# Optimization experiments

Measured on AMD Instinct MI355X. Metric: run time of the kernel, lower is better.

## Reference

```python
import jax, jax.numpy as jnp
import numpy as np

RATE = 0.1
RANDOM_PORTION = 0.1


def setup_inputs() -> dict:
    key = jax.random.key(0)
    x = jax.random.normal(key, (32, 524288), dtype=jnp.float32)
    return {"x": x}


def reference(x) -> jnp.ndarray:
    # Training-mode forward of RandomTopKModifier.
    b = x.shape[0]
    xf = x.reshape(b, -1)                      # [B, N]
    n = xf.shape[1]
    k = max(1, round(RATE * n))

    # 1) top-k by magnitude (indices only; unsorted is fine, set-equivalent)
    _, topk_idx = jax.lax.top_k(jnp.abs(xf), k)            # [B, k] int32

    # 2) build per-element sampling probabilities:
    #    random_portion mass spread over the N-k non-topk slots,
    #    (1 - random_portion) mass spread over the k topk slots.
    rows = jnp.arange(b)[:, None]                           # [B, 1]
    probs = jnp.full_like(xf, RANDOM_PORTION / (n - k))
    probs = probs.at[rows, topk_idx].set((1.0 - RANDOM_PORTION) / k)

    # 3) weighted sampling of k indices WITHOUT replacement
    #    (torch.multinomial(probs, k)) via the Gumbel-top-k trick.
    g = jax.random.gumbel(jax.random.key(42), xf.shape, dtype=xf.dtype)
    _, sel_idx = jax.lax.top_k(jnp.log(probs) + g, k)       # [B, k]

    # 4) scatter a binary mask and apply it
    mask = jnp.zeros_like(xf).at[rows, sel_idx].set(1.0)
    return (mask * xf).reshape(x.shape)
```

## Files before the change

### kernel.cpp

```cpp
#include <hip/hip_runtime.h>
#include <stdint.h>


static constexpr uint32_t BB = 32;
static constexpr uint32_t NN = 524288;
static constexpr uint32_t KK = 52429;
static constexpr uint32_t W = 64;
static constexpr uint32_t CHUNK = NN / W;
static constexpr uint32_t SEGCAP1 = 1024;
static constexpr uint32_t CAP1 = W * SEGCAP1;
static constexpr uint32_t SEGCAP2 = 1280;
static constexpr uint32_t CAP2 = W * SEGCAP2;
static constexpr uint32_t SELCAP = 512;
static constexpr uint32_t SENT = 0xFFFFFFFFu;
static constexpr uint32_t T1KEY = 0x3FD00000u;

__device__ __forceinline__ float xla_logf(float xin) {
#pragma clang fp contract(off)
  float x = fmaxf(xin, __uint_as_float(0x00800000u));
  uint32_t bits = __float_as_uint(x);
  float e = (float)((int)(bits >> 23) - 126);
  x = __uint_as_float((bits & 0x807fffffu) | 0x3f000000u);
  bool mlt = x < 0.707106781186547524f;
  float tmp = mlt ? x : 0.0f;
  x = x - 1.0f;
  e = e - (mlt ? 1.0f : 0.0f);
  x = x + tmp;
  float x2 = x * x;
  float x3 = x2 * x;
  float y, y1, y2;
  y  = 7.0376836292E-2f * x + -1.1514610310E-1f;
  y1 = -1.2420140846E-1f * x + 1.4249322787E-1f;
  y2 = 2.0000714765E-1f * x + -2.4999993993E-1f;
  y  = y * x + 1.1676998740E-1f;
  y1 = y1 * x + -1.6668057665E-1f;
  y2 = y2 * x + 3.3333331174E-1f;
  y  = y * x3 + y1;
  y  = y * x3 + y2;
  y  = y * x3;
  y1 = e * -2.12194440e-4f;
  tmp = x2 * 0.5f;
  y = y + y1;
  x = x - tmp;
  y2 = e * 0.693359375f;
  x = x + y;
  x = x + y2;
  return x;
}

__device__ __forceinline__ float c_top_val()  { return xla_logf((float)((1.0 - 0.1) / 52429.0)); }
__device__ __forceinline__ float c_rand_val() { return xla_logf((float)(0.1 / 471859.0)); }

__device__ __forceinline__ uint32_t tf_bits(uint32_t i) {
  const uint32_t ks0 = 0u, ks1 = 42u, ks2 = 0x1BD11BDAu ^ 42u;
  uint32_t x0 = 0u + ks0;
  uint32_t x1 = i + ks1;
#define TFR(r) { x0 += x1; x1 = (x1 << (r)) | (x1 >> (32 - (r))); x1 ^= x0; }
  TFR(13) TFR(15) TFR(26) TFR(6)
  x0 += ks1; x1 += ks2 + 1u;
  TFR(17) TFR(29) TFR(16) TFR(24)
  x0 += ks2; x1 += ks0 + 2u;
  TFR(13) TFR(15) TFR(26) TFR(6)
  x0 += ks0; x1 += ks1 + 3u;
  TFR(17) TFR(29) TFR(16) TFR(24)
  x0 += ks1; x1 += ks2 + 4u;
  TFR(13) TFR(15) TFR(26) TFR(6)
  x0 += ks2; x1 += ks0 + 5u;
#undef TFR
  return x0 ^ x1;
}

__device__ __forceinline__ uint32_t key_x(float v) { return __float_as_uint(v) & 0x7fffffffu; }
__device__ __forceinline__ uint32_t key_s(float v) {
  uint32_t b = __float_as_uint(v);
  return (b & 0x80000000u) ? ~b : (b | 0x80000000u);
}


__global__ void __launch_bounds__(256)
k_candcoll1(const float* __restrict__ src,
            uint32_t* __restrict__ cidx, uint32_t* __restrict__ ckey) {
  __shared__ uint32_t lcnt;
  uint32_t row = blockIdx.y, seg = blockIdx.x;
  if (threadIdx.x == 0) lcnt = 0u;
  __syncthreads();
  uint32_t colbase = seg * CHUNK;
  uint32_t base = row * CAP1 + seg * SEGCAP1;
  const float4* p = (const float4*)(src + (size_t)row * NN + colbase);
  for (uint32_t j = threadIdx.x; j < CHUNK / 4; j += 256) {
    float4 v = p[j];
    float vv[4] = {v.x, v.y, v.z, v.w};
#pragma unroll
    for (int e = 0; e < 4; ++e) {
      uint32_t key = key_x(vv[e]);
      if (key >= T1KEY) {
        uint32_t li = atomicAdd(&lcnt, 1u);
        if (li < SEGCAP1) { cidx[base + li] = colbase + j * 4 + e; ckey[base + li] = key; }
      }
    }
  }
  __syncthreads();
  uint32_t c = (lcnt < SEGCAP1) ? lcnt : SEGCAP1;
  for (uint32_t j = c + threadIdx.x; j < SEGCAP1; j += 256) ckey[base + j] = SENT;
}

__device__ __forceinline__ void scan_hist(const uint32_t* lh, uint32_t* csA,
                                          uint32_t* sh, uint32_t kk, uint32_t t) {
  uint32_t s0 = 0;
  if (t < 256) {
#pragma unroll
    for (int j = 0; j < 8; ++j) s0 += lh[t * 8 + j];
    csA[t] = s0;
  }
  __syncthreads();
#pragma unroll
  for (uint32_t stp = 1; stp < 256; stp <<= 1) {
    uint32_t v = 0;
    if (t < 256 && t + stp < 256) v = csA[t + stp];
    __syncthreads();
    if (t < 256) csA[t] += v;
    __syncthreads();
  }
  if (t < 256) {
    uint32_t Sst = csA[t] - s0;
    if (Sst < kk && Sst + s0 >= kk) {
      uint32_t acc = Sst, bin = t * 8;
      for (int b2 = (int)t * 8 + 7; b2 >= (int)t * 8; --b2) {
        uint32_t hv = lh[b2];
        if (acc + hv >= kk) { bin = (uint32_t)b2; break; }
        acc += hv;
      }
      sh[0] = bin; sh[1] = kk - acc;
    }
  }
  __syncthreads();
}

__global__ void __launch_bounds__(1024)
k_select(const uint32_t* __restrict__ cidx, const uint32_t* __restrict__ ckey,
         uint32_t cap, uint32_t* __restrict__ st, uint32_t* __restrict__ sel) {
  __shared__ uint32_t lh[2048];
  __shared__ uint32_t csA[256];
  __shared__ uint32_t lkey[1024];
  __shared__ uint32_t lidx[1024];
  __shared__ uint32_t sh[8];
  uint32_t row = blockIdx.x;
  uint32_t t = threadIdx.x;
  const uint4* pk = (const uint4*)(ckey + (size_t)row * cap);
  for (uint32_t b = t; b < 2048; b += 1024) lh[b] = 0u;
  __syncthreads();
  for (uint32_t j0 = 0; j0 < cap / 4; j0 += 4 * 1024) {
    uint4 k4[4];
#pragma unroll
    for (int u = 0; u < 4; ++u) k4[u] = pk[j0 + u * 1024 + t];
#pragma unroll
    for (int u = 0; u < 4; ++u) {
      uint32_t kk[4] = {k4[u].x, k4[u].y, k4[u].z, k4[u].w};
#pragma unroll
      for (int e = 0; e < 4; ++e)
        if (kk[e] != SENT) atomicAdd(&lh[kk[e] >> 21], 1u);
    }
  }
  __syncthreads();
  scan_hist(lh, csA, sh, KK, t);
  uint32_t b0 = sh[0], kk1 = sh[1];
  __syncthreads();
  for (uint32_t b = t; b < 2048; b += 1024) lh[b] = 0u;
  __syncthreads();
  for (uint32_t j0 = 0; j0 < cap / 4; j0 += 4 * 1024) {
    uint4 k4[4];
#pragma unroll
    for (int u = 0; u < 4; ++u) k4[u] = pk[j0 + u * 1024 + t];
#pragma unroll
    for (int u = 0; u < 4; ++u) {
      uint32_t kk[4] = {k4[u].x, k4[u].y, k4[u].z, k4[u].w};
#pragma unroll
      for (int e = 0; e < 4; ++e)
        if (kk[e] != SENT && (kk[e] >> 21) == b0)
          atomicAdd(&lh[(kk[e] >> 10) & 2047u], 1u);
    }
  }
  __syncthreads();
  scan_hist(lh, csA, sh, kk1, t);
  uint32_t p21 = (b0 << 11) | sh[0];
  uint32_t kk2 = sh[1];
  if (t == 0) sh[4] = 0u;
  __syncthreads();
  for (uint32_t j0 = 0; j0 < cap / 4; j0 += 4 * 1024) {
    uint4 k4[4];
#pragma unroll
    for (int u = 0; u < 4; ++u) k4[u] = pk[j0 + u * 1024 + t];
#pragma unroll
    for (int u = 0; u < 4; ++u) {
      uint32_t kk[4] = {k4[u].x, k4[u].y, k4[u].z, k4[u].w};
#pragma unroll
      for (int e = 0; e < 4; ++e) {
        if ((kk[e] >> 10) == p21) {
          uint32_t li = atomicAdd(&sh[4], 1u);
          if (li < 1024) { lkey[li] = kk[e]; lidx[li] = cidx[(size_t)row * cap + (j0 + u * 1024 + t) * 4 + e]; }
        }
      }
    }
  }
  __syncthreads();
  uint32_t cnt = sh[4]; if (cnt > 1024) cnt = 1024;
  if (t < cnt) {
    uint32_t myk = lkey[t], myi = lidx[t];
    uint32_t gt = 0, eq = 0, eqlt = 0;
    for (uint32_t b = 0; b < cnt; ++b) {
      uint32_t kb = lkey[b];
      gt += (kb > myk) ? 1u : 0u;
      if (kb == myk) { eq++; eqlt += (lidx[b] < myi) ? 1u : 0u; }
    }
    if (gt < kk2 && gt + eq >= kk2) {
      uint32_t m = kk2 - gt;
      if (eqlt == 0) { st[row * 8 + 2] = myk; st[row * 8 + 4] = (m > SELCAP) ? SELCAP : m; }
      if (eqlt < m && eqlt < SELCAP) sel[row * SELCAP + eqlt] = myi;
    }
  }
}

__global__ void __launch_bounds__(256)
k_compute_u(const float* __restrict__ x, const uint32_t* __restrict__ st1,
            const uint32_t* __restrict__ sel1,
            uint32_t* __restrict__ cidx, uint32_t* __restrict__ ckey) {
  __shared__ uint32_t lcnt;
  uint32_t row = blockIdx.y, seg = blockIdx.x;
  if (threadIdx.x == 0) lcnt = 0u;
  __syncthreads();
  uint32_t thr1 = st1[row * 8 + 2];
  uint32_t m1 = st1[row * 8 + 4];
  uint32_t colbase = seg * CHUNK;
  uint32_t base = row * CAP2 + seg * SEGCAP2;
  uint32_t ibase = (row << 19) + colbase;
  const float4* px = (const float4*)(x + (size_t)row * NN + colbase);
  for (uint32_t j = threadIdx.x; j < CHUNK / 4; j += 256) {
    float4 v = px[j];
    float vv[4] = {v.x, v.y, v.z, v.w};
#pragma unroll
    for (int e = 0; e < 4; ++e) {
      uint32_t col = colbase + j * 4 + e;
      uint32_t key = key_x(vv[e]);
      bool istop = key > thr1;
      if (key == thr1) {
        for (uint32_t q = 0; q < m1; ++q)
          if (sel1[row * SELCAP + q] == col) { istop = true; break; }
      }
      uint32_t b = tf_bits(ibase + j * 4 + e);
      float u = __uint_as_float((b >> 9) | 0x3f800000u) - 1.0f;
      u = fmaxf(u, 1.17549435e-38f);
      float bound = istop ? 0.150f : 0.9765f;
      if (u >= bound) {
        uint32_t li = atomicAdd(&lcnt, 1u);
        if (li < SEGCAP2) {
          cidx[base + li] = col | (istop ? 0x80000000u : 0u);
          ckey[base + li] = __float_as_uint(u);
        }
      }
    }
  }
  __syncthreads();
  uint32_t c = (lcnt < SEGCAP2) ? lcnt : SEGCAP2;
  for (uint32_t j = c + threadIdx.x; j < SEGCAP2; j += 256) ckey[base + j] = SENT;
}

__global__ void __launch_bounds__(256)
k_finish(uint32_t* __restrict__ cidx, uint32_t* __restrict__ ckey) {
  uint32_t row = blockIdx.y, seg = blockIdx.x;
  uint32_t base = row * CAP2 + seg * SEGCAP2;
  float CT = c_top_val(), CR = c_rand_val();
  for (uint32_t j = threadIdx.x; j < SEGCAP2; j += 256) {
    uint32_t ub = ckey[base + j];
    if (ub == SENT) continue;
    uint32_t ci = cidx[base + j];
    float u = __uint_as_float(ub);
    float nl = -xla_logf(u);
    float g = -xla_logf(nl);
    float s = ((ci >> 31) ? CT : CR) + g;
    ckey[base + j] = key_s(s);
    cidx[base + j] = ci & 0x7FFFFFFFu;
  }
}

__global__ void __launch_bounds__(256)
k_scatter(const float* __restrict__ x, float* __restrict__ out,
          const uint32_t* __restrict__ cidx, const uint32_t* __restrict__ ckey,
          const uint32_t* __restrict__ st2, const uint32_t* __restrict__ sel2) {
  uint32_t row = blockIdx.y, seg = blockIdx.x;
  uint32_t thr2 = st2[row * 8 + 2];
  uint32_t m2 = st2[row * 8 + 4];
  uint32_t base = row * CAP2 + seg * SEGCAP2;
  for (uint32_t j = threadIdx.x; j < SEGCAP2; j += 256) {
    uint32_t key = ckey[base + j];
    if (key == SENT) continue;
    uint32_t col = cidx[base + j];
    bool take = key > thr2;
    if (key == thr2) {
      for (uint32_t q = 0; q < m2; ++q)
        if (sel2[row * SELCAP + q] == col) { take = true; break; }
    }
    if (take) out[(size_t)row * NN + col] = x[(size_t)row * NN + col];
  }
}

extern "C" void kernel_launch(void* const* d_in, const int* in_sizes, int n_in,
                              void* d_out, int out_size, void* d_ws, size_t ws_size,
                              hipStream_t stream) {
  const float* x = (const float*)d_in[0];
  float* out = (float*)d_out;

  uint32_t* w = (uint32_t*)d_ws;
  uint32_t* st1   = w;
  uint32_t* st2   = st1 + BB * 8;
  uint32_t* sel1  = st2 + BB * 8;
  uint32_t* sel2  = sel1 + BB * SELCAP;
  uint32_t* cidx  = sel2 + BB * SELCAP;
  uint32_t* ckey  = cidx + BB * CAP2;

  dim3 blk(256), blkS(1024), gridF(W, BB), gridR(BB);

  k_candcoll1<<<gridF, blk, 0, stream>>>(x, cidx, ckey);
  k_select<<<gridR, blkS, 0, stream>>>(cidx, ckey, CAP1, st1, sel1);

  k_compute_u<<<gridF, blk, 0, stream>>>(x, st1, sel1, cidx, ckey);

  k_finish<<<gridF, blk, 0, stream>>>(cidx, ckey);

  k_select<<<gridR, blkS, 0, stream>>>(cidx, ckey, CAP2, st2, sel2);

  hipMemsetAsync(out, 0, (size_t)BB * NN * 4u, stream);
  k_scatter<<<gridF, blk, 0, stream>>>(x, out, cidx, ckey, st2, sel2);
}
```

Before: 182.8 us.

## Use wave-aggregated atomics and single-pass offset histogram in select

Candidate collection in both filtering kernels now uses wave ballot plus a single leader atomic per wavefront instead of per-element shared atomics. The select kernel replaces its two-level radix histogram with one histogram of fine bins offset by a known lower bound, dropping one full pass over the candidate keys. The uniform-threshold compare is done on raw integer bits, with the float conversion moved to the finish kernel and sentinels now also marked in the index array. The risk is that the clamped top bin or an overfull bin (more than 1024 keys) could break exactness if the key distribution is wider than assumed.

```diff
diff --git a/kernel.cpp b/kernel.cpp
--- a/kernel.cpp
+++ b/kernel.cpp
@@ -14,6 +14,8 @@
 static constexpr uint32_t SELCAP = 512;
 static constexpr uint32_t SENT = 0xFFFFFFFFu;
 static constexpr uint32_t T1KEY = 0x3FD00000u;
+static constexpr uint32_t LO1 = T1KEY;
+static constexpr uint32_t LO2 = 0x3EC4CCCCu;
 
 __device__ __forceinline__ float xla_logf(float xin) {
 #pragma clang fp contract(off)
@@ -84,6 +86,7 @@
   uint32_t row = blockIdx.y, seg = blockIdx.x;
   if (threadIdx.x == 0) lcnt = 0u;
   __syncthreads();
+  uint32_t lane = threadIdx.x & 63u;
   uint32_t colbase = seg * CHUNK;
   uint32_t base = row * CAP1 + seg * SEGCAP1;
   const float4* p = (const float4*)(src + (size_t)row * NN + colbase);
@@ -93,9 +96,17 @@
 #pragma unroll
     for (int e = 0; e < 4; ++e) {
       uint32_t key = key_x(vv[e]);
-      if (key >= T1KEY) {
-        uint32_t li = atomicAdd(&lcnt, 1u);
-        if (li < SEGCAP1) { cidx[base + li] = colbase + j * 4 + e; ckey[base + li] = key; }
+      bool cand = (key >= T1KEY);
+      unsigned long long bal = __ballot(cand);
+      if (bal) {
+        uint32_t leader = (uint32_t)__ffsll((long long)bal) - 1u;
+        uint32_t bw = 0;
+        if (lane == leader) bw = atomicAdd(&lcnt, (uint32_t)__popcll(bal));
+        bw = __shfl(bw, (int)leader);
+        if (cand) {
+          uint32_t li = bw + (uint32_t)__popcll(bal & ((1ull << lane) - 1ull));
+          if (li < SEGCAP1) { cidx[base + li] = colbase + j * 4 + e; ckey[base + li] = key; }
+        }
       }
     }
   }
@@ -138,7 +149,7 @@
 
 __global__ void __launch_bounds__(1024)
 k_select(const uint32_t* __restrict__ cidx, const uint32_t* __restrict__ ckey,
-         uint32_t cap, uint32_t* __restrict__ st, uint32_t* __restrict__ sel) {
+         uint32_t cap, uint32_t LO, uint32_t* __restrict__ st, uint32_t* __restrict__ sel) {
   __shared__ uint32_t lh[2048];
   __shared__ uint32_t csA[256];
   __shared__ uint32_t lkey[1024];
@@ -157,15 +168,19 @@
     for (int u = 0; u < 4; ++u) {
       uint32_t kk[4] = {k4[u].x, k4[u].y, k4[u].z, k4[u].w};
 #pragma unroll
-      for (int e = 0; e < 4; ++e)
-        if (kk[e] != SENT) atomicAdd(&lh[kk[e] >> 21], 1u);
+      for (int e = 0; e < 4; ++e) {
+        if (kk[e] != SENT) {
+          uint32_t bin = (kk[e] - LO) >> 13;
+          if (bin > 2047u) bin = 2047u;
+          atomicAdd(&lh[bin], 1u);
+        }
+      }
     }
   }
   __syncthreads();
   scan_hist(lh, csA, sh, KK, t);
-  uint32_t b0 = sh[0], kk1 = sh[1];
-  __syncthreads();
-  for (uint32_t b = t; b < 2048; b += 1024) lh[b] = 0u;
+  uint32_t bstar = sh[0], kkW = sh[1];
+  if (t == 0) sh[4] = 0u;
   __syncthreads();
   for (uint32_t j0 = 0; j0 < cap / 4; j0 += 4 * 1024) {
     uint4 k4[4];
@@ -175,27 +190,8 @@
     for (int u = 0; u < 4; ++u) {
       uint32_t kk[4] = {k4[u].x, k4[u].y, k4[u].z, k4[u].w};
 #pragma unroll
-      for (int e = 0; e < 4; ++e)
-        if (kk[e] != SENT && (kk[e] >> 21) == b0)
-          atomicAdd(&lh[(kk[e] >> 10) & 2047u], 1u);
-    }
-  }
-  __syncthreads();
-  scan_hist(lh, csA, sh, kk1, t);
-  uint32_t p21 = (b0 << 11) | sh[0];
-  uint32_t kk2 = sh[1];
-  if (t == 0) sh[4] = 0u;
-  __syncthreads();
-  for (uint32_t j0 = 0; j0 < cap / 4; j0 += 4 * 1024) {
-    uint4 k4[4];
-#pragma unroll
-    for (int u = 0; u < 4; ++u) k4[u] = pk[j0 + u * 1024 + t];
-#pragma unroll
-    for (int u = 0; u < 4; ++u) {
-      uint32_t kk[4] = {k4[u].x, k4[u].y, k4[u].z, k4[u].w};
-#pragma unroll
       for (int e = 0; e < 4; ++e) {
-        if ((kk[e] >> 10) == p21) {
+        if (kk[e] != SENT && ((kk[e] - LO) >> 13) == bstar) {
           uint32_t li = atomicAdd(&sh[4], 1u);
           if (li < 1024) { lkey[li] = kk[e]; lidx[li] = cidx[(size_t)row * cap + (j0 + u * 1024 + t) * 4 + e]; }
         }
@@ -212,8 +208,8 @@
       gt += (kb > myk) ? 1u : 0u;
       if (kb == myk) { eq++; eqlt += (lidx[b] < myi) ? 1u : 0u; }
     }
-    if (gt < kk2 && gt + eq >= kk2) {
-      uint32_t m = kk2 - gt;
+    if (gt < kkW && gt + eq >= kkW) {
+      uint32_t m = kkW - gt;
       if (eqlt == 0) { st[row * 8 + 2] = myk; st[row * 8 + 4] = (m > SELCAP) ? SELCAP : m; }
       if (eqlt < m && eqlt < SELCAP) sel[row * SELCAP + eqlt] = myi;
     }
@@ -228,6 +224,9 @@
   uint32_t row = blockIdx.y, seg = blockIdx.x;
   if (threadIdx.x == 0) lcnt = 0u;
   __syncthreads();
+  const uint32_t BT = (uint32_t)ceilf(0.150f  * 8388608.0f) << 9;
+  const uint32_t BR = (uint32_t)ceilf(0.9765f * 8388608.0f) << 9;
+  uint32_t lane = threadIdx.x & 63u;
   uint32_t thr1 = st1[row * 8 + 2];
   uint32_t m1 = st1[row * 8 + 4];
   uint32_t colbase = seg * CHUNK;
@@ -247,21 +246,29 @@
           if (sel1[row * SELCAP + q] == col) { istop = true; break; }
       }
       uint32_t b = tf_bits(ibase + j * 4 + e);
-      float u = __uint_as_float((b >> 9) | 0x3f800000u) - 1.0f;
-      u = fmaxf(u, 1.17549435e-38f);
-      float bound = istop ? 0.150f : 0.9765f;
-      if (u >= bound) {
-        uint32_t li = atomicAdd(&lcnt, 1u);
-        if (li < SEGCAP2) {
-          cidx[base + li] = col | (istop ? 0x80000000u : 0u);
-          ckey[base + li] = __float_as_uint(u);
+      bool cand = (b >= (istop ? BT : BR));
+      unsigned long long bal = __ballot(cand);
+      if (bal) {
+        uint32_t leader = (uint32_t)__ffsll((long long)bal) - 1u;
+        uint32_t bw = 0;
+        if (lane == leader) bw = atomicAdd(&lcnt, (uint32_t)__popcll(bal));
+        bw = __shfl(bw, (int)leader);
+        if (cand) {
+          uint32_t li = bw + (uint32_t)__popcll(bal & ((1ull << lane) - 1ull));
+          if (li < SEGCAP2) {
+            cidx[base + li] = col | (istop ? 0x80000000u : 0u);
+            ckey[base + li] = b;
+          }
         }
       }
     }
   }
   __syncthreads();
   uint32_t c = (lcnt < SEGCAP2) ? lcnt : SEGCAP2;
-  for (uint32_t j = c + threadIdx.x; j < SEGCAP2; j += 256) ckey[base + j] = SENT;
+  for (uint32_t j = c + threadIdx.x; j < SEGCAP2; j += 256) {
+    cidx[base + j] = SENT;
+    ckey[base + j] = SENT;
+  }
 }
 
 __global__ void __launch_bounds__(256)
@@ -270,10 +277,11 @@
   uint32_t base = row * CAP2 + seg * SEGCAP2;
   float CT = c_top_val(), CR = c_rand_val();
   for (uint32_t j = threadIdx.x; j < SEGCAP2; j += 256) {
-    uint32_t ub = ckey[base + j];
-    if (ub == SENT) continue;
     uint32_t ci = cidx[base + j];
-    float u = __uint_as_float(ub);
+    if (ci == SENT) continue;
+    uint32_t b = ckey[base + j];
+    float u = __uint_as_float((b >> 9) | 0x3f800000u) - 1.0f;
+    u = fmaxf(u, 1.17549435e-38f);
     float nl = -xla_logf(u);
     float g = -xla_logf(nl);
     float s = ((ci >> 31) ? CT : CR) + g;
@@ -320,13 +328,13 @@
   dim3 blk(256), blkS(1024), gridF(W, BB), gridR(BB);
 
   k_candcoll1<<<gridF, blk, 0, stream>>>(x, cidx, ckey);
-  k_select<<<gridR, blkS, 0, stream>>>(cidx, ckey, CAP1, st1, sel1);
+  k_select<<<gridR, blkS, 0, stream>>>(cidx, ckey, CAP1, LO1, st1, sel1);
 
   k_compute_u<<<gridF, blk, 0, stream>>>(x, st1, sel1, cidx, ckey);
 
   k_finish<<<gridF, blk, 0, stream>>>(cidx, ckey);
 
-  k_select<<<gridR, blkS, 0, stream>>>(cidx, ckey, CAP2, st2, sel2);
+  k_select<<<gridR, blkS, 0, stream>>>(cidx, ckey, CAP2, LO2, st2, sel2);
 
   hipMemsetAsync(out, 0, (size_t)BB * NN * 4u, stream);
   k_scatter<<<gridF, blk, 0, stream>>>(x, out, cidx, ckey, st2, sel2);
```

New measurement: 155.0 us. 1.18x faster.
